# Performance work log

Hardware: AMD Instinct MI355X
Metric: run time of the kernel (lower is better)

## Reference

```python
import jax, jax.numpy as jnp
import numpy as np

THRESHOLD = 0.5
NEG_POS = 3
ALPHA = 0.5
EPS = 1e-6


def cxcy2xy(b):
    return jnp.concatenate([b[:, :2] - b[:, 2:] / 2, b[:, :2] + b[:, 2:] / 2], axis=1)


def xy2cxcy(b):
    return jnp.concatenate([(b[:, 2:] + b[:, :2]) / 2, b[:, 2:] - b[:, :2]], axis=1)


def encode_boxes(b, d):
    return jnp.concatenate([(b[:, :2] - d[:, :2]) / (d[:, 2:] / 10 + EPS),
                            jnp.log(b[:, 2:] / d[:, 2:] + EPS) * 5], axis=1)


def find_iou(a, b):
    # a: [O,4] xy, b: [N,4] xy -> [O,N]
    lt = jnp.maximum(a[:, None, :2], b[None, :, :2])
    rb = jnp.minimum(a[:, None, 2:], b[None, :, 2:])
    wh = jnp.clip(rb - lt, 0.0)
    inter = wh[..., 0] * wh[..., 1]
    area_a = (a[:, 2] - a[:, 0]) * (a[:, 3] - a[:, 1])
    area_b = (b[:, 2] - b[:, 0]) * (b[:, 3] - b[:, 1])
    return inter / (area_a[:, None] + area_b[None, :] - inter)


def _match(boxes_i, labels_i, def_xy, default_boxes):
    # boxes_i: [O,4] xy, labels_i: [O], def_xy/default_boxes: [N,4]
    n_obj = boxes_i.shape[0]
    overlap = find_iou(boxes_i, def_xy)            # [O, N]
    overlap_defbox = overlap.max(axis=0)           # [N]
    object_defbox = overlap.argmax(axis=0)         # [N]
    defbox_object = overlap.argmax(axis=1)         # [O]
    object_defbox = object_defbox.at[defbox_object].set(jnp.arange(n_obj))
    overlap_defbox = overlap_defbox.at[defbox_object].set(1.0)
    label = labels_i[object_defbox]
    label = jnp.where(overlap_defbox < THRESHOLD, 0, label)
    t_loc = encode_boxes(xy2cxcy(boxes_i[object_defbox]), default_boxes)
    return t_loc, label


def reference(locs_pred, cls_pred, boxes, labels, default_boxes):
    B, N, C = cls_pred.shape
    def_xy = cxcy2xy(default_boxes)
    t_locs, t_classes = jax.vmap(_match, in_axes=(0, 0, None, None))(
        boxes, labels, def_xy, default_boxes)      # [B,N,4], [B,N]

    pos = t_classes != 0                            # [B,N]
    n_pos = pos.sum(axis=1)                         # [B]
    n_pos_total = n_pos.sum().astype(jnp.float32)

    # SmoothL1 (beta=1), mean over positive-box coordinate elements
    d = jnp.abs(locs_pred - t_locs)
    sl1 = jnp.where(d < 1.0, 0.5 * d * d, d - 0.5)
    loc_loss = jnp.sum(sl1 * pos[..., None].astype(sl1.dtype)) / (n_pos_total * 4.0)

    # per-anchor cross entropy
    logp = jax.nn.log_softmax(cls_pred, axis=-1)
    all_conf = -jnp.take_along_axis(logp, t_classes[..., None], axis=-1)[..., 0]  # [B,N]

    pos_conf = jnp.sum(jnp.where(pos, all_conf, 0.0))
    neg_conf = jnp.where(pos, 0.0, all_conf)
    neg_sorted = -jnp.sort(-neg_conf, axis=1)       # descending
    hard = jnp.arange(N)[None, :] < (NEG_POS * n_pos)[:, None]
    hard_sum = jnp.sum(jnp.where(hard, neg_sorted, 0.0))

    conf_loss = (hard_sum + pos_conf) / n_pos_total
    return ALPHA * loc_loss + conf_loss


def setup_inputs() -> dict:
    key = jax.random.key(0)
    k1, k2, k3, k4, k5, k6, k7 = jax.random.split(key, 7)
    B, N, C, O = 32, 24564, 81, 16
    locs_pred = jax.random.normal(k1, (B, N, 4), dtype=jnp.float32)
    cls_pred = jax.random.normal(k2, (B, N, C), dtype=jnp.float32)
    # ground-truth boxes: valid xy boxes inside [0,1]
    cxy = jax.random.uniform(k3, (B, O, 2), minval=0.2, maxval=0.8)
    wh = jax.random.uniform(k4, (B, O, 2), minval=0.05, maxval=0.3)
    boxes = jnp.concatenate([cxy - wh / 2, cxy + wh / 2], axis=-1).astype(jnp.float32)
    labels = jax.random.randint(k5, (B, O), 1, C)
    dcxy = jax.random.uniform(k6, (N, 2), minval=0.05, maxval=0.95)
    dwh = jax.random.uniform(k7, (N, 2), minval=0.05, maxval=0.4)
    default_boxes = jnp.concatenate([dcxy, dwh], axis=-1).astype(jnp.float32)
    return {"locs_pred": locs_pred, "cls_pred": cls_pred, "boxes": boxes,
            "labels": labels, "default_boxes": default_boxes}
```

## Files before the change

kernel.cpp:

```cpp
#include <hip/hip_runtime.h>
#include <math.h>

#define THRESH    0.5f
#define NEG_POSK  3
#define EPSf      1e-6f
#define CCLS      81
#define TILEA     64
#define CHUNKS    16
#define TPB       16

__device__ __forceinline__ float iou_xy(float ax0, float ay0, float ax1, float ay1,
                                        float bx0, float by0, float bx1, float by1) {
    float lx = fmaxf(ax0, bx0), ly = fmaxf(ay0, by0);
    float rx = fminf(ax1, bx1), ry = fminf(ay1, by1);
    float w = fmaxf(rx - lx, 0.f), h = fmaxf(ry - ly, 0.f);
    float inter = w * h;
    float aa = (ax1 - ax0) * (ay1 - ay0);
    float ab = (bx1 - bx0) * (by1 - by0);
    return inter / (aa + ab - inter);
}

__device__ __forceinline__ void gload16(const void* g, void* l) {
    __builtin_amdgcn_global_load_lds(
        (const __attribute__((address_space(1))) void*)g,
        (__attribute__((address_space(3))) void*)l, 16, 0, 0);
}

__global__ __launch_bounds__(256) void k_obj_part(const float* __restrict__ boxes,
                                                  const float* __restrict__ dboxes,
                                                  float* __restrict__ part_iou,
                                                  int* __restrict__ part_idx,
                                                  int N, int O) {
    int bo = blockIdx.x;
    int c  = blockIdx.y;
    const float* bb = boxes + (size_t)bo * 4;
    float ax0 = bb[0], ay0 = bb[1], ax1 = bb[2], ay1 = bb[3];
    int chunk = (N + CHUNKS - 1) / CHUNKS;
    int n0 = c * chunk;
    int n1 = min(n0 + chunk, N);
    float best = -1.f; int bi = 0x7FFFFFFF;
    for (int n = n0 + threadIdx.x; n < n1; n += 256) {
        float4 d = ((const float4*)dboxes)[n];
        float dx0 = d.x - d.z * 0.5f, dy0 = d.y - d.w * 0.5f;
        float dx1 = d.x + d.z * 0.5f, dy1 = d.y + d.w * 0.5f;
        float iou = iou_xy(ax0, ay0, ax1, ay1, dx0, dy0, dx1, dy1);
        if (iou > best) { best = iou; bi = n; }
    }
    #pragma unroll
    for (int dd = 1; dd < 64; dd <<= 1) {
        float v2 = __shfl_xor(best, dd); int i2 = __shfl_xor(bi, dd);
        if (v2 > best || (v2 == best && i2 < bi)) { best = v2; bi = i2; }
    }
    __shared__ float sv[4]; __shared__ int si[4];
    int w = threadIdx.x >> 6;
    if ((threadIdx.x & 63) == 0) { sv[w] = best; si[w] = bi; }
    __syncthreads();
    if (threadIdx.x == 0) {
        #pragma unroll
        for (int i = 1; i < 4; ++i)
            if (sv[i] > best || (sv[i] == best && si[i] < bi)) { best = sv[i]; bi = si[i]; }
        part_iou[(size_t)bo * CHUNKS + c] = best;
        part_idx[(size_t)bo * CHUNKS + c] = bi;
    }
}

__global__ void k_obj_reduce(const float* __restrict__ part_iou,
                             const int* __restrict__ part_idx,
                             int* __restrict__ defbox_object, int BO) {
    int bo = blockIdx.x * blockDim.x + threadIdx.x;
    if (bo >= BO) return;
    float best = -1.f; int bi = 0x7FFFFFFF;
    #pragma unroll
    for (int c = 0; c < CHUNKS; ++c) {
        float v = part_iou[(size_t)bo * CHUNKS + c];
        int  i = part_idx[(size_t)bo * CHUNKS + c];
        if (v > best || (v == best && i < bi)) { best = v; bi = i; }
    }
    defbox_object[bo] = bi;
}

template<int OT>
__global__ __launch_bounds__(256)
void k_conf(const float* __restrict__ locs_pred,
            const float* __restrict__ cls,
            const float* __restrict__ boxes,
            const int* __restrict__ labels,
            const float* __restrict__ dboxes,
            const int* __restrict__ dbo_g,
            float* __restrict__ vneg,
            int* __restrict__ n_pos,
            float* __restrict__ loc_sum,
            float* __restrict__ pos_conf,
            int N, int O_rt, int bpb, int tilesPerBatch, long long maxF4) {
    const int O = OT ? OT : O_rt;
    __shared__ __align__(16) float sm[4][2][16 * CCLS];
    __shared__ float sbb[64];
    __shared__ int slab[16], sdbo[16];
    __shared__ float swl[4], swp[4];
    __shared__ int swc[4];
    const int tid = threadIdx.x;
    const int b  = blockIdx.x / bpb;
    const int t0 = (blockIdx.x % bpb) * TPB;
    const int tEnd = min(t0 + TPB, tilesPerBatch);

    if (tid < O * 4) sbb[tid] = boxes[(size_t)b * O * 4 + tid];
    else if (tid < O * 5) slab[tid - O * 4] = labels[(size_t)b * O + tid - O * 4];
    else if (tid < O * 6) sdbo[tid - O * 5] = dbo_g[(size_t)b * O + tid - O * 5];

    const int lane = tid & 63, w = tid >> 6;
    const int j = lane & 15, q = lane >> 4;

    auto stage = [&](int buf, int t) {
        long long base4 = (((long long)b * N + (long long)t * TILEA + w * 16)
                           * CCLS) >> 2;
        const float4* g4 = (const float4*)cls;
        float4* s4 = (float4*)&sm[w][buf][0];
        #pragma unroll
        for (int k2 = 0; k2 < 5; ++k2) {
            long long gi = base4 + k2 * 64 + lane;
            if (gi > maxF4) gi = maxF4;
            gload16(g4 + gi, s4 + k2 * 64);
        }
        if (lane < 4) {
            long long gi = base4 + 320 + lane;
            if (gi > maxF4) gi = maxF4;
            gload16(g4 + gi, s4 + 320);
        }
    };

    stage(0, t0);
    __syncthreads();

    float obx0[4], oby0[4], obx1[4], oby1[4], oarea[4];
    int odbo[4];
    #pragma unroll
    for (int oo = 0; oo < 4; ++oo) {
        int o = q * 4 + oo;
        obx0[oo] = sbb[o*4];   oby0[oo] = sbb[o*4+1];
        obx1[oo] = sbb[o*4+2]; oby1[oo] = sbb[o*4+3];
        oarea[oo] = (obx1[oo] - obx0[oo]) * (oby1[oo] - oby0[oo]);
        odbo[oo] = sdbo[o];
    }

    float pc = 0.f, ls = 0.f; int cnt = 0;

    auto phase2 = [&](int buf, int t) {
        int a0 = t * TILEA;
        int valid = min(TILEA, N - a0);
        int a = w * 16 + j;
        bool act = a < valid;
        int n = a0 + a;
        int nc = min(n, N - 1);
        float4 d = ((const float4*)dboxes)[nc];
        float dx0 = d.x - d.z * 0.5f, dy0 = d.y - d.w * 0.5f;
        float dx1 = d.x + d.z * 0.5f, dy1 = d.y + d.w * 0.5f;
        float areaD = d.z * d.w;
        float bi = -1.f, bu = 1.f; int bsel = q * 4;
        int fs = -1;
        #pragma unroll
        for (int oo = 0; oo < 4; ++oo) {
            float lx = fmaxf(obx0[oo], dx0), ly = fmaxf(oby0[oo], dy0);
            float rx = fminf(obx1[oo], dx1), ry = fminf(oby1[oo], dy1);
            float ww = fmaxf(rx - lx, 0.f), hh = fmaxf(ry - ly, 0.f);
            float inter = ww * hh;
            float uni = oarea[oo] + areaD - inter;
            float c1 = inter * bu, c2 = bi * uni;
            if (c1 > c2) { bi = inter; bu = uni; bsel = q * 4 + oo; }
            if (odbo[oo] == n) fs = q * 4 + oo;
        }
        #pragma unroll
        for (int dd = 16; dd < 64; dd <<= 1) {
            float oi = __shfl_xor(bi, dd), ou = __shfl_xor(bu, dd);
            int os = __shfl_xor(bsel, dd);
            int of = __shfl_xor(fs, dd);
            float c1 = oi * bu, c2 = bi * ou;
            if (c1 > c2 || (c1 == c2 && os < bsel)) { bi = oi; bu = ou; bsel = os; }
            fs = max(fs, of);
        }
        const float* row = &sm[w][buf][j * CCLS];
        float s = 0.f;
        if (act) {
            int c0 = q * 20;
            #pragma unroll
            for (int i = 0; i < 20; ++i) s += __expf(row[c0 + i]);
            if (q == 3) s += __expf(row[80]);
        }
        s += __shfl_xor(s, 16);
        s += __shfl_xor(s, 32);
        if (act && q == 0) {
            bool forced = fs >= 0;
            int sel = forced ? fs : bsel;
            bool meets = forced || (bi >= 0.5f * bu);
            int lbl = meets ? slab[sel] : 0;
            float conf = __logf(s) - row[lbl];
            bool pos = (lbl != 0);
            size_t idx = (size_t)b * N + n;
            float4 p = ((const float4*)locs_pred)[idx];
            vneg[idx] = pos ? 0.f : conf;
            if (pos) {
                pc += conf; cnt++;
                float bx0 = sbb[sel*4], by0 = sbb[sel*4+1];
                float bx1 = sbb[sel*4+2], by1 = sbb[sel*4+3];
                float bcx = (bx0 + bx1) * 0.5f, bcy = (by0 + by1) * 0.5f;
                float bw = bx1 - bx0, bh = by1 - by0;
                float t0f = (bcx - d.x) / (d.z / 10.0f + EPSf);
                float t1f = (bcy - d.y) / (d.w / 10.0f + EPSf);
                float t2f = __logf(bw / d.z + EPSf) * 5.0f;
                float t3f = __logf(bh / d.w + EPSf) * 5.0f;
                float dd;
                dd = fabsf(p.x - t0f); ls += (dd < 1.f) ? 0.5f*dd*dd : dd - 0.5f;
                dd = fabsf(p.y - t1f); ls += (dd < 1.f) ? 0.5f*dd*dd : dd - 0.5f;
                dd = fabsf(p.z - t2f); ls += (dd < 1.f) ? 0.5f*dd*dd : dd - 0.5f;
                dd = fabsf(p.w - t3f); ls += (dd < 1.f) ? 0.5f*dd*dd : dd - 0.5f;
            }
        }
    };

    int cur = 0;
    for (int t = t0; t < tEnd; ++t) {
        bool has_next = (t + 1 < tEnd);
        if (has_next) stage(cur ^ 1, t + 1);
        if (t == t0)
            asm volatile("s_waitcnt vmcnt(6)" ::: "memory");
        else if (has_next)
            asm volatile("s_waitcnt vmcnt(9)" ::: "memory");
        else
            asm volatile("s_waitcnt vmcnt(3)" ::: "memory");
        phase2(cur, t);
        cur ^= 1;
    }

    #pragma unroll
    for (int dd = 1; dd < 64; dd <<= 1) {
        pc  += __shfl_xor(pc, dd);
        ls  += __shfl_xor(ls, dd);
        cnt += __shfl_xor(cnt, dd);
    }
    if (lane == 0) { swp[w] = pc; swl[w] = ls; swc[w] = cnt; }
    __syncthreads();
    if (tid == 0) {
        float P = swp[0] + swp[1] + swp[2] + swp[3];
        float L = swl[0] + swl[1] + swl[2] + swl[3];
        int   C = swc[0] + swc[1] + swc[2] + swc[3];
        if (C) {
            atomicAdd(&n_pos[b], C);
            atomicAdd(loc_sum, L);
            atomicAdd(pos_conf, P);
        }
    }
}

__device__ void wave_select(const int* hist, int nbins, int k, int* out_bin, int* out_k) {
    int lane = threadIdx.x & 63;
    int cum = 0;
    for (int c = nbins / 64 - 1; c >= 0; --c) {
        int val = hist[c * 64 + lane];
        int s = val;
        for (int d = 1; d < 64; d <<= 1) {
            int t = __shfl_down(s, d);
            if (lane + d < 64) s += t;
        }
        int total = __shfl(s, 0);
        if (cum + total >= k) {
            unsigned long long mask = __ballot(cum + s >= k);
            int bl = 63 - __builtin_clzll(mask);
            int sB = __shfl(s, bl);
            int vB = __shfl(val, bl);
            if (lane == 0) {
                *out_bin = c * 64 + bl;
                *out_k = k - (cum + sB - vB);
            }
            return;
        }
        cum += total;
    }
    if (lane == 0) { *out_bin = 0; *out_k = 1; }
}

__global__ __launch_bounds__(1024) void k_select(const float* __restrict__ vneg,
                                                 const int* __restrict__ n_pos,
                                                 float* __restrict__ hard_sum,
                                                 int B, int N) {
    int b = blockIdx.x;
    const float* v = vneg + (size_t)b * N;
    __shared__ int hist[2048];
    __shared__ int bcast_bin, bcast_k;
    __shared__ float swv[16];
    __shared__ int swc[16];
    int np = n_pos[b];
    long long kk = (long long)NEG_POSK * np;
    if (kk > N) kk = N;
    int k = (int)kk;
    if (k <= 0) return;
    int tid = threadIdx.x;

    for (int i = tid; i < 2048; i += 1024) hist[i] = 0;
    __syncthreads();
    for (int n = tid; n < N; n += 1024) {
        unsigned u = __float_as_uint(v[n]);
        atomicAdd(&hist[u >> 20], 1);
    }
    __syncthreads();
    if (tid < 64) wave_select(hist, 2048, k, &bcast_bin, &bcast_k);
    __syncthreads();
    int B1 = bcast_bin, k2 = bcast_k;

    for (int i = tid; i < 2048; i += 1024) hist[i] = 0;
    __syncthreads();
    for (int n = tid; n < N; n += 1024) {
        unsigned u = __float_as_uint(v[n]);
        if ((int)(u >> 20) == B1) atomicAdd(&hist[(u >> 9) & 0x7FF], 1);
    }
    __syncthreads();
    if (tid < 64) wave_select(hist, 2048, k2, &bcast_bin, &bcast_k);
    __syncthreads();
    int B2 = bcast_bin, k3 = bcast_k;
    unsigned pre = ((unsigned)B1 << 11) | (unsigned)B2;

    for (int i = tid; i < 512; i += 1024) hist[i] = 0;
    __syncthreads();
    for (int n = tid; n < N; n += 1024) {
        unsigned u = __float_as_uint(v[n]);
        if ((u >> 9) == pre) atomicAdd(&hist[u & 0x1FF], 1);
    }
    __syncthreads();
    if (tid < 64) wave_select(hist, 512, k3, &bcast_bin, &bcast_k);
    __syncthreads();
    unsigned tau_bits = (pre << 9) | (unsigned)bcast_bin;
    float tau = __uint_as_float(tau_bits);

    float ssum = 0.f; int scnt = 0;
    for (int n = tid; n < N; n += 1024) {
        float x = v[n];
        if (x > tau) { ssum += x; scnt++; }
    }
    for (int d = 1; d < 64; d <<= 1) {
        ssum += __shfl_xor(ssum, d);
        scnt += __shfl_xor(scnt, d);
    }
    int w = tid >> 6;
    if ((tid & 63) == 0) { swv[w] = ssum; swc[w] = scnt; }
    __syncthreads();
    if (tid == 0) {
        float S = 0.f; int Ct = 0;
        for (int i = 0; i < 16; ++i) { S += swv[i]; Ct += swc[i]; }
        float hb = S + (float)(k - Ct) * tau;
        atomicAdd(hard_sum, hb);
    }
}

__global__ void k_final(const int* __restrict__ n_pos,
                        const float* __restrict__ loc_sum,
                        const float* __restrict__ pos_conf,
                        const float* __restrict__ hard_sum,
                        float* __restrict__ out, int B) {
    if (threadIdx.x == 0 && blockIdx.x == 0) {
        int tot = 0;
        for (int b = 0; b < B; ++b) tot += n_pos[b];
        float np = (float)tot;
        float loc = *loc_sum / (np * 4.0f);
        float conf = (*hard_sum + *pos_conf) / np;
        out[0] = 0.5f * loc + conf;
    }
}

extern "C" void kernel_launch(void* const* d_in, const int* in_sizes, int n_in,
                              void* d_out, int out_size, void* d_ws, size_t ws_size,
                              hipStream_t stream) {
    const float* locs_pred = (const float*)d_in[0];
    const float* cls_pred  = (const float*)d_in[1];
    const float* boxes     = (const float*)d_in[2];
    const int*   labels    = (const int*)d_in[3];
    const float* dboxes    = (const float*)d_in[4];

    int N = in_sizes[4] / 4;
    int B = in_sizes[0] / (4 * N);
    int O = in_sizes[3] / B;
    int BO = B * O;

    size_t BN = (size_t)B * N;
    char* ws = (char*)d_ws;
    int*   n_pos    = (int*)ws;
    float* loc_sum  = (float*)(ws + 128);
    float* pos_conf = (float*)(ws + 132);
    float* hard_sum = (float*)(ws + 136);
    float* vneg     = (float*)(ws + 256);
    int*   defbox_object = (int*)(ws + 256 + BN * 4);
    float* part_iou = (float*)(ws + 256 + BN * 4 + (size_t)BO * 4);
    int*   part_idx = (int*)(part_iou + (size_t)BO * CHUNKS);

    hipMemsetAsync(ws, 0, 256, stream);

    dim3 gop(BO, CHUNKS);
    k_obj_part<<<gop, 256, 0, stream>>>(boxes, dboxes, part_iou, part_idx, N, O);
    k_obj_reduce<<<(BO + 255) / 256, 256, 0, stream>>>(part_iou, part_idx,
                                                       defbox_object, BO);
    int tilesPerBatch = (N + TILEA - 1) / TILEA;
    int bpb = (tilesPerBatch + TPB - 1) / TPB;
    long long maxF4 = (((long long)B * N * CCLS) >> 2) - 1;
    dim3 gc(B * bpb);
    if (O == 16)
        k_conf<16><<<gc, 256, 0, stream>>>(locs_pred, cls_pred, boxes, labels, dboxes,
                                           defbox_object, vneg, n_pos, loc_sum,
                                           pos_conf, N, O, bpb, tilesPerBatch, maxF4);
    else
        k_conf<0><<<gc, 256, 0, stream>>>(locs_pred, cls_pred, boxes, labels, dboxes,
                                          defbox_object, vneg, n_pos, loc_sum,
                                          pos_conf, N, O, bpb, tilesPerBatch, maxF4);
    k_select<<<B, 1024, 0, stream>>>(vneg, n_pos, hard_sum, B, N);
    k_final<<<1, 1, 0, stream>>>(n_pos, loc_sum, pos_conf, hard_sum, (float*)d_out, B);
}
```

Before: 124.1 us.

## Shrink k_conf to single-wave blocks over 16-anchor slabs

Restructures the confidence kernel so each block is one 64-thread wave that streams 16 consecutive 16-anchor slabs of class logits, instead of four waves each owning part of a 64-anchor tile. This drops the cross-wave shared-memory reduction and __syncthreads, and quadruples the block count, which should improve load balance and latency hiding. The locs_pred load is also hoisted earlier so it overlaps with the IoU work. The cost is more blocks, each with less work, and four times as many atomics to the global accumulators.

```diff
diff --git a/kernel.cpp b/kernel.cpp
--- a/kernel.cpp
+++ b/kernel.cpp
@@ -5,9 +5,8 @@
 #define NEG_POSK  3
 #define EPSf      1e-6f
 #define CCLS      81
-#define TILEA     64
 #define CHUNKS    16
-#define TPB       16
+#define SPB       16
 
 __device__ __forceinline__ float iou_xy(float ax0, float ay0, float ax1, float ay1,
                                         float bx0, float by0, float bx1, float by1) {
@@ -80,7 +79,7 @@
 }
 
 template<int OT>
-__global__ __launch_bounds__(256)
+__global__ __launch_bounds__(64)
 void k_conf(const float* __restrict__ locs_pred,
             const float* __restrict__ cls,
             const float* __restrict__ boxes,
@@ -91,30 +90,35 @@
             int* __restrict__ n_pos,
             float* __restrict__ loc_sum,
             float* __restrict__ pos_conf,
-            int N, int O_rt, int bpb, int tilesPerBatch, long long maxF4) {
+            int N, int O_rt, int bpb, int nSlabs, long long maxF4) {
     const int O = OT ? OT : O_rt;
-    __shared__ __align__(16) float sm[4][2][16 * CCLS];
+    __shared__ __align__(16) float sm[2][16 * CCLS];
     __shared__ float sbb[64];
     __shared__ int slab[16], sdbo[16];
-    __shared__ float swl[4], swp[4];
-    __shared__ int swc[4];
     const int tid = threadIdx.x;
     const int b  = blockIdx.x / bpb;
-    const int t0 = (blockIdx.x % bpb) * TPB;
-    const int tEnd = min(t0 + TPB, tilesPerBatch);
-
-    if (tid < O * 4) sbb[tid] = boxes[(size_t)b * O * 4 + tid];
-    else if (tid < O * 5) slab[tid - O * 4] = labels[(size_t)b * O + tid - O * 4];
-    else if (tid < O * 6) sdbo[tid - O * 5] = dbo_g[(size_t)b * O + tid - O * 5];
-
-    const int lane = tid & 63, w = tid >> 6;
+    const int s0 = (blockIdx.x % bpb) * SPB;
+    const int sEnd = min(s0 + SPB, nSlabs);
+
+    if (OT == 16) {
+        sbb[tid] = boxes[(size_t)b * 64 + tid];
+        if (tid < 16) slab[tid] = labels[(size_t)b * 16 + tid];
+        else if (tid < 32) sdbo[tid - 16] = dbo_g[(size_t)b * 16 + tid - 16];
+    } else {
+        for (int i = tid; i < O * 4; i += 64) sbb[i] = boxes[(size_t)b * O * 4 + i];
+        for (int i = tid; i < O; i += 64) {
+            slab[i] = labels[(size_t)b * O + i];
+            sdbo[i] = dbo_g[(size_t)b * O + i];
+        }
+    }
+
+    const int lane = tid;
     const int j = lane & 15, q = lane >> 4;
 
-    auto stage = [&](int buf, int t) {
-        long long base4 = (((long long)b * N + (long long)t * TILEA + w * 16)
-                           * CCLS) >> 2;
+    auto stage = [&](int buf, int s) {
+        long long base4 = (((long long)b * N + (long long)s * 16) * CCLS) >> 2;
         const float4* g4 = (const float4*)cls;
-        float4* s4 = (float4*)&sm[w][buf][0];
+        float4* s4 = (float4*)&sm[buf][0];
         #pragma unroll
         for (int k2 = 0; k2 < 5; ++k2) {
             long long gi = base4 + k2 * 64 + lane;
@@ -128,7 +132,7 @@
         }
     };
 
-    stage(0, t0);
+    stage(0, s0);
     __syncthreads();
 
     float obx0[4], oby0[4], obx1[4], oby1[4], oarea[4];
@@ -136,22 +140,28 @@
     #pragma unroll
     for (int oo = 0; oo < 4; ++oo) {
         int o = q * 4 + oo;
-        obx0[oo] = sbb[o*4];   oby0[oo] = sbb[o*4+1];
-        obx1[oo] = sbb[o*4+2]; oby1[oo] = sbb[o*4+3];
+        if (OT == 16 || o < O) {
+            obx0[oo] = sbb[o*4];   oby0[oo] = sbb[o*4+1];
+            obx1[oo] = sbb[o*4+2]; oby1[oo] = sbb[o*4+3];
+            odbo[oo] = sdbo[o];
+        } else {
+            obx0[oo] = 1e30f; oby0[oo] = 1e30f; obx1[oo] = 1e30f; oby1[oo] = 1e30f;
+            odbo[oo] = -1;
+        }
         oarea[oo] = (obx1[oo] - obx0[oo]) * (oby1[oo] - oby0[oo]);
-        odbo[oo] = sdbo[o];
     }
 
     float pc = 0.f, ls = 0.f; int cnt = 0;
 
-    auto phase2 = [&](int buf, int t) {
-        int a0 = t * TILEA;
-        int valid = min(TILEA, N - a0);
-        int a = w * 16 + j;
-        bool act = a < valid;
-        int n = a0 + a;
+    auto phase2 = [&](int buf, int s) {
+        int n = s * 16 + j;
+        bool act = n < N;
         int nc = min(n, N - 1);
+        size_t idx = (size_t)b * N + nc;
         float4 d = ((const float4*)dboxes)[nc];
+        float4 p;
+        if (act && q == 0)
+            p = ((const float4*)locs_pred)[idx];
         float dx0 = d.x - d.z * 0.5f, dy0 = d.y - d.w * 0.5f;
         float dx1 = d.x + d.z * 0.5f, dy1 = d.y + d.w * 0.5f;
         float areaD = d.z * d.w;
@@ -177,25 +187,23 @@
             if (c1 > c2 || (c1 == c2 && os < bsel)) { bi = oi; bu = ou; bsel = os; }
             fs = max(fs, of);
         }
-        const float* row = &sm[w][buf][j * CCLS];
-        float s = 0.f;
+        const float* row = &sm[buf][j * CCLS];
+        float s_ = 0.f;
         if (act) {
             int c0 = q * 20;
             #pragma unroll
-            for (int i = 0; i < 20; ++i) s += __expf(row[c0 + i]);
-            if (q == 3) s += __expf(row[80]);
-        }
-        s += __shfl_xor(s, 16);
-        s += __shfl_xor(s, 32);
+            for (int i = 0; i < 20; ++i) s_ += __expf(row[c0 + i]);
+            if (q == 3) s_ += __expf(row[80]);
+        }
+        s_ += __shfl_xor(s_, 16);
+        s_ += __shfl_xor(s_, 32);
         if (act && q == 0) {
             bool forced = fs >= 0;
             int sel = forced ? fs : bsel;
             bool meets = forced || (bi >= 0.5f * bu);
             int lbl = meets ? slab[sel] : 0;
-            float conf = __logf(s) - row[lbl];
+            float conf = __logf(s_) - row[lbl];
             bool pos = (lbl != 0);
-            size_t idx = (size_t)b * N + n;
-            float4 p = ((const float4*)locs_pred)[idx];
             vneg[idx] = pos ? 0.f : conf;
             if (pos) {
                 pc += conf; cnt++;
@@ -207,26 +215,26 @@
                 float t1f = (bcy - d.y) / (d.w / 10.0f + EPSf);
                 float t2f = __logf(bw / d.z + EPSf) * 5.0f;
                 float t3f = __logf(bh / d.w + EPSf) * 5.0f;
-                float dd;
-                dd = fabsf(p.x - t0f); ls += (dd < 1.f) ? 0.5f*dd*dd : dd - 0.5f;
-                dd = fabsf(p.y - t1f); ls += (dd < 1.f) ? 0.5f*dd*dd : dd - 0.5f;
-                dd = fabsf(p.z - t2f); ls += (dd < 1.f) ? 0.5f*dd*dd : dd - 0.5f;
-                dd = fabsf(p.w - t3f); ls += (dd < 1.f) ? 0.5f*dd*dd : dd - 0.5f;
+                float dd2;
+                dd2 = fabsf(p.x - t0f); ls += (dd2 < 1.f) ? 0.5f*dd2*dd2 : dd2 - 0.5f;
+                dd2 = fabsf(p.y - t1f); ls += (dd2 < 1.f) ? 0.5f*dd2*dd2 : dd2 - 0.5f;
+                dd2 = fabsf(p.z - t2f); ls += (dd2 < 1.f) ? 0.5f*dd2*dd2 : dd2 - 0.5f;
+                dd2 = fabsf(p.w - t3f); ls += (dd2 < 1.f) ? 0.5f*dd2*dd2 : dd2 - 0.5f;
             }
         }
     };
 
     int cur = 0;
-    for (int t = t0; t < tEnd; ++t) {
-        bool has_next = (t + 1 < tEnd);
-        if (has_next) stage(cur ^ 1, t + 1);
-        if (t == t0)
+    for (int s = s0; s < sEnd; ++s) {
+        bool has_next = (s + 1 < sEnd);
+        if (has_next) stage(cur ^ 1, s + 1);
+        if (s == s0)
             asm volatile("s_waitcnt vmcnt(6)" ::: "memory");
         else if (has_next)
             asm volatile("s_waitcnt vmcnt(9)" ::: "memory");
         else
             asm volatile("s_waitcnt vmcnt(3)" ::: "memory");
-        phase2(cur, t);
+        phase2(cur, s);
         cur ^= 1;
     }
 
@@ -236,17 +244,10 @@
         ls  += __shfl_xor(ls, dd);
         cnt += __shfl_xor(cnt, dd);
     }
-    if (lane == 0) { swp[w] = pc; swl[w] = ls; swc[w] = cnt; }
-    __syncthreads();
-    if (tid == 0) {
-        float P = swp[0] + swp[1] + swp[2] + swp[3];
-        float L = swl[0] + swl[1] + swl[2] + swl[3];
-        int   C = swc[0] + swc[1] + swc[2] + swc[3];
-        if (C) {
-            atomicAdd(&n_pos[b], C);
-            atomicAdd(loc_sum, L);
-            atomicAdd(pos_conf, P);
-        }
+    if (lane == 0 && cnt) {
+        atomicAdd(&n_pos[b], cnt);
+        atomicAdd(loc_sum, ls);
+        atomicAdd(pos_conf, pc);
     }
 }
 
@@ -395,18 +396,18 @@
     k_obj_part<<<gop, 256, 0, stream>>>(boxes, dboxes, part_iou, part_idx, N, O);
     k_obj_reduce<<<(BO + 255) / 256, 256, 0, stream>>>(part_iou, part_idx,
                                                        defbox_object, BO);
-    int tilesPerBatch = (N + TILEA - 1) / TILEA;
-    int bpb = (tilesPerBatch + TPB - 1) / TPB;
+    int nSlabs = (N + 15) / 16;
+    int bpb = (nSlabs + SPB - 1) / SPB;
     long long maxF4 = (((long long)B * N * CCLS) >> 2) - 1;
     dim3 gc(B * bpb);
     if (O == 16)
-        k_conf<16><<<gc, 256, 0, stream>>>(locs_pred, cls_pred, boxes, labels, dboxes,
-                                           defbox_object, vneg, n_pos, loc_sum,
-                                           pos_conf, N, O, bpb, tilesPerBatch, maxF4);
+        k_conf<16><<<gc, 64, 0, stream>>>(locs_pred, cls_pred, boxes, labels, dboxes,
+                                          defbox_object, vneg, n_pos, loc_sum,
+                                          pos_conf, N, O, bpb, nSlabs, maxF4);
     else
-        k_conf<0><<<gc, 256, 0, stream>>>(locs_pred, cls_pred, boxes, labels, dboxes,
-                                          defbox_object, vneg, n_pos, loc_sum,
-                                          pos_conf, N, O, bpb, tilesPerBatch, maxF4);
+        k_conf<0><<<gc, 64, 0, stream>>>(locs_pred, cls_pred, boxes, labels, dboxes,
+                                         defbox_object, vneg, n_pos, loc_sum,
+                                         pos_conf, N, O, bpb, nSlabs, maxF4);
     k_select<<<B, 1024, 0, stream>>>(vneg, n_pos, hard_sum, B, N);
     k_final<<<1, 1, 0, stream>>>(n_pos, loc_sum, pos_conf, hard_sum, (float*)d_out, B);
 }
```

Result: slower. 184.9 us (+49.0%).
